# Kernel tuning notes

Hardware: AMD Instinct MI355X
Metric: run time of the kernel (lower is better)

## Reference

```python
import jax, jax.numpy as jnp
import numpy as np

B_, C_, NH_, WS_, HID_ = 8, 512, 16, 7, 2048
HH, WW = 56, 56


def _rel_pos_index(ws):
    coords = np.stack(np.meshgrid(np.arange(ws), np.arange(ws), indexing='ij'))  # (2,ws,ws)
    cf = coords.reshape(2, -1)
    rc = (cf[:, :, None] - cf[:, None, :]).transpose(1, 2, 0)  # (ws2,ws2,2)
    rc[..., 0] += ws - 1
    rc[..., 1] += ws - 1
    rc[..., 0] *= 2 * ws - 1
    return jnp.asarray(rc.sum(-1).reshape(-1))  # (ws2*ws2,)


def _ln(x, g, b, eps):
    mu = x.mean(-1, keepdims=True)
    var = ((x - mu) ** 2).mean(-1, keepdims=True)
    return (x - mu) * jax.lax.rsqrt(var + eps) * g + b


def setup_inputs() -> dict:
    key = jax.random.key(0)
    ks = jax.random.split(key, 8)
    s = lambda k, shape: (jax.random.normal(k, shape, jnp.float32) * 0.02)
    return {
        'x': jax.random.normal(ks[0], (B_, HH * WW, C_), jnp.float32),
        'H': HH, 'W': WW,
        'norm1_g': jnp.ones((C_,), jnp.float32), 'norm1_b': jnp.zeros((C_,), jnp.float32),
        'norm2_g': jnp.ones((C_,), jnp.float32), 'norm2_b': jnp.zeros((C_,), jnp.float32),
        'qkv_w': s(ks[1], (3 * C_, C_)), 'qkv_b': jnp.zeros((3 * C_,), jnp.float32),
        'rpb': s(ks[2], ((2 * WS_ - 1) ** 2, NH_)),
        'fc1_w': s(ks[3], (HID_, C_)), 'fc1_b': jnp.zeros((HID_,), jnp.float32),
        'dw_w': s(ks[4], (HID_, 1, 3, 3)), 'dw_b': jnp.zeros((HID_,), jnp.float32),
        'fc2_w': s(ks[5], (C_, HID_)), 'fc2_b': jnp.zeros((C_,), jnp.float32),
    }


def reference(x, H, W, norm1_g, norm1_b, norm2_g, norm2_b, qkv_w, qkv_b, rpb,
              fc1_w, fc1_b, dw_w, dw_b, fc2_w, fc2_b):
    B, N, C = x.shape
    ws, nh = WS_, NH_
    hd = C // nh
    scale = hd ** -0.5
    ws2 = ws * ws
    nHw, nWw = H // ws, W // ws

    # ---- norm1 + WaveAttention (windowed attention w/ relative position bias) ----
    h = _ln(x, norm1_g, norm1_b, 1e-5)
    qkv = h @ qkv_w.T + qkv_b                                   # [B,N,3C]
    # window partition: [B, nH, ws, nW, ws, 3, nh, hd] -> [3, B*nH*nW, nh, ws2, hd]
    qkv = qkv.reshape(B, nHw, ws, nWw, ws, 3, nh, hd)
    qkv = qkv.transpose(5, 0, 1, 3, 6, 2, 4, 7).reshape(3, B * nHw * nWw, nh, ws2, hd)
    q, k, v = qkv[0], qkv[1], qkv[2]

    attn = jnp.einsum('wnid,wnjd->wnij', q, k) * scale          # [Bw,nh,ws2,ws2]
    bias = rpb[_rel_pos_index(ws)].reshape(ws2, ws2, nh).transpose(2, 0, 1)
    attn = jax.nn.softmax(attn + bias[None], axis=-1)
    out = jnp.einsum('wnij,wnjd->wnid', attn, v)                # [Bw,nh,ws2,hd]
    # window reverse
    out = out.transpose(0, 2, 1, 3).reshape(B, nHw, nWw, ws, ws, C)
    out = out.transpose(0, 1, 3, 2, 4, 5).reshape(B, N, C)
    x = x + out

    # ---- norm2 + PVT2FFN (fc1 -> depthwise 3x3 conv -> GELU -> fc2) ----
    h2 = _ln(x, norm2_g, norm2_b, 1e-5)
    h2 = h2 @ fc1_w.T + fc1_b                                   # [B,N,HID]
    img = h2.reshape(B, H, W, HID_).transpose(0, 3, 1, 2)       # [B,HID,H,W]
    img = jax.lax.conv_general_dilated(img, dw_w, (1, 1), 'SAME',
                                       feature_group_count=HID_)
    img = img + dw_b[None, :, None, None]
    h2 = img.reshape(B, HID_, N).transpose(0, 2, 1)
    h2 = jax.nn.gelu(h2, approximate=False)
    h2 = h2 @ fc2_w.T + fc2_b
    return x + h2
```

## Files before the change

kernel.cpp:

```cpp
#include <hip/hip_runtime.h>
#include <hip/hip_bf16.h>

typedef unsigned short u16;
typedef unsigned int u32;
typedef __attribute__((ext_vector_type(8))) short bf16x8_t;
typedef __attribute__((ext_vector_type(4))) float f32x4_t;
typedef __attribute__((ext_vector_type(8))) u16 u16x8;
typedef __attribute__((ext_vector_type(4))) u32 u32x4;

constexpr int B_  = 8;
constexpr int C_  = 512;
constexpr int NH_ = 16;
constexpr int HID_= 2048;
constexpr int Hh  = 56, Ww = 56;
constexpr int N_  = Hh * Ww;
constexpr int M_  = B_ * N_;

__device__ __forceinline__ u16 f2bf(float f) {
    u32 u = __float_as_uint(f);
    u32 r = (u + 0x7fffu + ((u >> 16) & 1u)) >> 16;
    return (u16)r;
}
__device__ __forceinline__ float bf2f(u16 v) {
    return __uint_as_float(((u32)v) << 16);
}

__device__ __forceinline__ void bar_raw() {
    __asm__ __volatile__("s_barrier" ::: "memory");
}

typedef const void __attribute__((address_space(1))) gvoid_t;
typedef void __attribute__((address_space(3))) lvoid_t;
__device__ __forceinline__ void gload16(const u16* g, u16* l) {
    __builtin_amdgcn_global_load_lds((gvoid_t*)g, (lvoid_t*)l, 16, 0, 0);
}

__global__ void cvt_w(const float* __restrict__ qkvw, const float* __restrict__ fc1w,
                      const float* __restrict__ fc2w, u16* __restrict__ oq,
                      u16* __restrict__ o1, u16* __restrict__ o2) {
    int i = blockIdx.x * 256 + threadIdx.x;
    if (i < 3 * C_ * C_) oq[i] = f2bf(qkvw[i]);
    if (i < HID_ * C_) { o1[i] = f2bf(fc1w[i]); o2[i] = f2bf(fc2w[i]); }
}

__global__ __launch_bounds__(256) void ln_kernel(const float* __restrict__ x,
        const float* __restrict__ g, const float* __restrict__ b, u16* __restrict__ out) {
    int lane = threadIdx.x & 63, wv = threadIdx.x >> 6;
    size_t row = (size_t)blockIdx.x * 4 + wv;
    const float4* xr = (const float4*)(x + row * C_);
    float4 a = xr[lane * 2], c = xr[lane * 2 + 1];
    float s  = a.x + a.y + a.z + a.w + c.x + c.y + c.z + c.w;
    float ss = a.x*a.x + a.y*a.y + a.z*a.z + a.w*a.w + c.x*c.x + c.y*c.y + c.z*c.z + c.w*c.w;
    #pragma unroll
    for (int off = 1; off < 64; off <<= 1) {
        s  += __shfl_xor(s, off);
        ss += __shfl_xor(ss, off);
    }
    float mean = s * (1.0f / C_);
    float var  = ss * (1.0f / C_) - mean * mean;
    float rstd = rsqrtf(var + 1e-5f);
    const float4* g4 = (const float4*)g;
    const float4* b4 = (const float4*)b;
    float4 g0 = g4[lane*2], g1 = g4[lane*2+1], b0 = b4[lane*2], b1 = b4[lane*2+1];
    u16x8 o;
    o[0] = f2bf((a.x - mean) * rstd * g0.x + b0.x);
    o[1] = f2bf((a.y - mean) * rstd * g0.y + b0.y);
    o[2] = f2bf((a.z - mean) * rstd * g0.z + b0.z);
    o[3] = f2bf((a.w - mean) * rstd * g0.w + b0.w);
    o[4] = f2bf((c.x - mean) * rstd * g1.x + b1.x);
    o[5] = f2bf((c.y - mean) * rstd * g1.y + b1.y);
    o[6] = f2bf((c.z - mean) * rstd * g1.z + b1.z);
    o[7] = f2bf((c.w - mean) * rstd * g1.w + b1.w);
    *(u16x8*)&out[row * C_ + lane * 8] = o;
}

template<bool RES, bool OUT_BF16>
__global__ __launch_bounds__(512) void gemm256(
        const u16* __restrict__ A, const u16* __restrict__ B,
        const float* __restrict__ bias, const float* __restrict__ res,
        void* __restrict__ Cout, int M, int N, int K,
        int nbm, int nbn) {
    const int nwg = nbm * nbn;
    const int id = blockIdx.x;
    const int xcd = id & 7, i = id >> 3;
    const int q = nwg >> 3, r = nwg & 7;
    const int gidx = (xcd < r ? xcd * (q + 1) : r * (q + 1) + (xcd - r) * q) + i;
    const int bm = gidx / nbn;
    const int bn = gidx - bm * nbn;

    __shared__ __align__(16) u16 As[2 * 16384];
    __shared__ __align__(16) u16 Bs[2 * 16384];
    const int tid = threadIdx.x;
    const int lane = tid & 63;
    const int w = tid >> 6;
    const int qr = w >> 1, qc = w & 1;

    const int r0 = lane >> 2;
    const int gcb = ((lane & 3) ^ ((lane >> 3) & 3));
    const int fr = lane & 15;
    const int g4 = lane >> 4;
    const int swz = (g4 ^ ((fr >> 1) & 3)) * 8;

    const u16* aBase = A + (size_t)(bm * 256) * K;
    const u16* bBase = B + (size_t)(bn * 256) * K;

    f32x4_t acc[2][2][2][4];
    f32x4_t zero = {0.f, 0.f, 0.f, 0.f};
    #pragma unroll
    for (int a0 = 0; a0 < 2; a0++)
        #pragma unroll
        for (int b0 = 0; b0 < 2; b0++)
            #pragma unroll
            for (int c0 = 0; c0 < 2; c0++)
                #pragma unroll
                for (int d0 = 0; d0 < 4; d0++) acc[a0][b0][c0][d0] = zero;

    auto stage = [&](const u16* gb, u16* lb, int u, int hf) {
        const u16* src = gb + (size_t)(hf * 128 + w * 16 + r0) * K
                            + (size_t)(u * 64 + gcb * 8);
        u16* dst = lb + (u & 1) * 16384 + hf * 8192 + w * 512;
        gload16(src, dst);
        gload16(src + 32, dst + 4096);
    };

    const int NT = K >> 6;
    stage(aBase, As, 0, 0);
    stage(bBase, Bs, 0, 0);
    stage(aBase, As, 0, 1);
    stage(bBase, Bs, 0, 1);
    stage(bBase, Bs, 1, 0);
    stage(aBase, As, 1, 0);
    __asm__ __volatile__("s_waitcnt vmcnt(4)" ::: "memory");
    bar_raw();

    for (int t = 0; t < NT; t++) {
        const int bb = (t & 1) * 16384;
        bf16x8_t bfv[2][4];
        #pragma unroll
        for (int pp = 0; pp < 4; pp++) {
            const int mh = pp & 1, nh = pp >> 1;
            bf16x8_t af[2][2];
            #pragma unroll
            for (int ks = 0; ks < 2; ks++)
                #pragma unroll
                for (int mf = 0; mf < 2; mf++)
                    af[ks][mf] = *(const bf16x8_t*)&As[bb + mh * 8192 + ks * 4096
                                    + (qr * 2 + mf) * 512 + fr * 32 + swz];
            if (pp == 0 || pp == 2) {
                #pragma unroll
                for (int ks = 0; ks < 2; ks++)
                    #pragma unroll
                    for (int nf = 0; nf < 4; nf++)
                        bfv[ks][nf] = *(const bf16x8_t*)&Bs[bb + nh * 8192 + ks * 4096
                                        + (qc * 4 + nf) * 512 + fr * 32 + swz];
            }
            if (pp == 0) {
                if (t + 1 < NT) stage(aBase, As, t + 1, 1);
            } else if (pp == 1) {
                if (t + 1 < NT) stage(bBase, Bs, t + 1, 1);
            } else if (pp == 2) {
                if (t + 2 < NT) stage(bBase, Bs, t + 2, 0);
            } else {
                if (t + 2 < NT) {
                    stage(aBase, As, t + 2, 0);
                    __asm__ __volatile__("s_waitcnt vmcnt(4)" ::: "memory");
                } else if (t + 1 < NT) {
                    __asm__ __volatile__("s_waitcnt vmcnt(0)" ::: "memory");
                }
            }
            bar_raw();
            __asm__ __volatile__("s_waitcnt lgkmcnt(0)" ::: "memory");
            __builtin_amdgcn_s_setprio(1);
            #pragma unroll
            for (int mf = 0; mf < 2; mf++)
                #pragma unroll
                for (int nf = 0; nf < 4; nf++)
                    #pragma unroll
                    for (int ks = 0; ks < 2; ks++)
                        acc[mh][nh][mf][nf] = __builtin_amdgcn_mfma_f32_16x16x32_bf16(
                            af[ks][mf], bfv[ks][nf], acc[mh][nh][mf][nf], 0, 0, 0);
            __builtin_amdgcn_s_setprio(0);
            bar_raw();
        }
    }

    #pragma unroll
    for (int mh = 0; mh < 2; mh++)
        #pragma unroll
        for (int nh = 0; nh < 2; nh++)
            #pragma unroll
            for (int mf = 0; mf < 2; mf++)
                #pragma unroll
                for (int rr = 0; rr < 4; rr++) {
                    int row = bm * 256 + mh * 128 + qr * 32 + mf * 16 + (lane >> 4) * 4 + rr;
                    #pragma unroll
                    for (int nf = 0; nf < 4; nf++) {
                        int col = bn * 256 + nh * 128 + qc * 64 + nf * 16 + (lane & 15);
                        float v = acc[mh][nh][mf][nf][rr] + bias[col];
                        if constexpr (RES) v += res[(size_t)row * N + col];
                        if constexpr (OUT_BF16) ((u16*)Cout)[(size_t)row * N + col] = f2bf(v);
                        else ((float*)Cout)[(size_t)row * N + col] = v;
                    }
                }
}

constexpr int QS = 40;
constexpr int VS = 72;
constexpr int PS = 72;

__global__ __launch_bounds__(256) void attn_kernel(
        const u16* __restrict__ qkv, const float* __restrict__ rpb,
        u16* __restrict__ aout) {
    __shared__ __align__(16) u16 q_s[64 * QS];
    __shared__ __align__(16) u16 k_s[64 * QS];
    __shared__ __align__(16) u16 vT_s[32 * VS];
    __shared__ __align__(16) u16 p_s[64 * PS];
    const int tid = threadIdx.x, lane = tid & 63, wv = tid >> 6;
    const int wh = blockIdx.x;
    const int head = wh & 15, w = wh >> 4;
    const int b = w >> 6, win = w & 63, bh = win >> 3, bw = win & 7;

    {
        int i = tid >> 2, dc = (tid & 3) * 8;
        if (i < 49) {
            int n = (bh * 7 + i / 7) * Ww + (bw * 7 + i % 7);
            const u16* base = qkv + ((size_t)(b * N_ + n)) * (3 * C_) + head * 32 + dc;
            *(u16x8*)&q_s[i * QS + dc] = *(const u16x8*)(base);
            *(u16x8*)&k_s[i * QS + dc] = *(const u16x8*)(base + C_);
        } else {
            u16x8 z = {0,0,0,0,0,0,0,0};
            *(u16x8*)&q_s[i * QS + dc] = z;
            *(u16x8*)&k_s[i * QS + dc] = z;
        }
    }
    for (int f = tid; f < 64 * 32; f += 256) {
        int i = f >> 5, d = f & 31;
        u16 val = 0;
        if (i < 49) {
            int n = (bh * 7 + i / 7) * Ww + (bw * 7 + i % 7);
            val = qkv[((size_t)(b * N_ + n)) * (3 * C_) + 2 * C_ + head * 32 + d];
        }
        vT_s[d * VS + i] = val;
    }
    __syncthreads();

    f32x4_t zero = {0.f, 0.f, 0.f, 0.f};
    f32x4_t s[4];
    bf16x8_t aq = *(const bf16x8_t*)&q_s[(wv * 16 + (lane & 15)) * QS + (lane >> 4) * 8];
    #pragma unroll
    for (int nt = 0; nt < 4; nt++) {
        bf16x8_t bk = *(const bf16x8_t*)&k_s[(nt * 16 + (lane & 15)) * QS + (lane >> 4) * 8];
        s[nt] = __builtin_amdgcn_mfma_f32_16x16x32_bf16(aq, bk, zero, 0, 0, 0);
    }

    const float scale = 0.17677669529663687f;
    #pragma unroll
    for (int r = 0; r < 4; r++) {
        int row = wv * 16 + (lane >> 4) * 4 + r;
        int qy = row / 7, qx = row - qy * 7;
        float pv[4];
        float m = -1e30f;
        #pragma unroll
        for (int nt = 0; nt < 4; nt++) {
            int col = nt * 16 + (lane & 15);
            float bias;
            if (row < 49 && col < 49) {
                int ky = col / 7, kx = col - ky * 7;
                bias = rpb[((qy - ky + 6) * 13 + (qx - kx + 6)) * NH_ + head];
            } else bias = -1e30f;
            float v = s[nt][r] * scale + bias;
            pv[nt] = v;
            m = fmaxf(m, v);
        }
        #pragma unroll
        for (int off = 1; off < 16; off <<= 1) m = fmaxf(m, __shfl_xor(m, off));
        float sum = 0.f;
        #pragma unroll
        for (int nt = 0; nt < 4; nt++) { pv[nt] = __expf(pv[nt] - m); sum += pv[nt]; }
        #pragma unroll
        for (int off = 1; off < 16; off <<= 1) sum += __shfl_xor(sum, off);
        float inv = 1.0f / sum;
        #pragma unroll
        for (int nt = 0; nt < 4; nt++)
            p_s[row * PS + nt * 16 + (lane & 15)] = f2bf(pv[nt] * inv);
    }
    __syncthreads();

    f32x4_t o[2] = {zero, zero};
    #pragma unroll
    for (int kt = 0; kt < 2; kt++) {
        bf16x8_t ap = *(const bf16x8_t*)&p_s[(wv * 16 + (lane & 15)) * PS + kt * 32 + (lane >> 4) * 8];
        #pragma unroll
        for (int nt = 0; nt < 2; nt++) {
            bf16x8_t bv = *(const bf16x8_t*)&vT_s[(nt * 16 + (lane & 15)) * VS + kt * 32 + (lane >> 4) * 8];
            o[nt] = __builtin_amdgcn_mfma_f32_16x16x32_bf16(ap, bv, o[nt], 0, 0, 0);
        }
    }
    u16* obase = aout + ((size_t)(w * 16 + head)) * 49 * 32;
    #pragma unroll
    for (int nt = 0; nt < 2; nt++) {
        #pragma unroll
        for (int r = 0; r < 4; r++) {
            int row = wv * 16 + (lane >> 4) * 4 + r;
            if (row < 49)
                obase[row * 32 + nt * 16 + (lane & 15)] = f2bf(o[nt][r]);
        }
    }
}

__global__ __launch_bounds__(256) void wrev_ln(const float* __restrict__ x,
        const u16* __restrict__ aout, const float* __restrict__ g,
        const float* __restrict__ bt, float* __restrict__ x2, u16* __restrict__ h) {
    int lane = threadIdx.x & 63, wvv = threadIdx.x >> 6;
    int m = blockIdx.x * 4 + wvv;
    int b = m / N_, n = m - b * N_;
    int iy = n / Ww, ix = n - iy * Ww;
    int w = b * 64 + (iy / 7) * 8 + (ix / 7);
    int pos = (iy % 7) * 7 + (ix % 7);
    int head = lane >> 2, d0 = (lane & 3) * 8;
    u16x8 ao = *(const u16x8*)&aout[(((size_t)w * 16 + head) * 49 + pos) * 32 + d0];
    const float4* xr = (const float4*)(x + (size_t)m * C_ + lane * 8);
    float4 a = xr[0], c = xr[1];
    float v[8];
    v[0] = a.x + bf2f(ao[0]); v[1] = a.y + bf2f(ao[1]);
    v[2] = a.z + bf2f(ao[2]); v[3] = a.w + bf2f(ao[3]);
    v[4] = c.x + bf2f(ao[4]); v[5] = c.y + bf2f(ao[5]);
    v[6] = c.z + bf2f(ao[6]); v[7] = c.w + bf2f(ao[7]);
    float s = 0.f, ss = 0.f;
    #pragma unroll
    for (int jj = 0; jj < 8; jj++) { s += v[jj]; ss += v[jj] * v[jj]; }
    #pragma unroll
    for (int off = 1; off < 64; off <<= 1) {
        s  += __shfl_xor(s, off);
        ss += __shfl_xor(ss, off);
    }
    float mean = s * (1.0f / C_);
    float var  = ss * (1.0f / C_) - mean * mean;
    float rstd = rsqrtf(var + 1e-5f);
    float4 o0 = {v[0], v[1], v[2], v[3]}, o1 = {v[4], v[5], v[6], v[7]};
    float4* x2r = (float4*)(x2 + (size_t)m * C_ + lane * 8);
    x2r[0] = o0; x2r[1] = o1;
    const float4* g4 = (const float4*)(g + lane * 8);
    const float4* b4 = (const float4*)(bt + lane * 8);
    float4 g0 = g4[0], g1 = g4[1], bb0 = b4[0], bb1 = b4[1];
    u16x8 o;
    o[0] = f2bf((v[0] - mean) * rstd * g0.x + bb0.x);
    o[1] = f2bf((v[1] - mean) * rstd * g0.y + bb0.y);
    o[2] = f2bf((v[2] - mean) * rstd * g0.z + bb0.z);
    o[3] = f2bf((v[3] - mean) * rstd * g0.w + bb0.w);
    o[4] = f2bf((v[4] - mean) * rstd * g1.x + bb1.x);
    o[5] = f2bf((v[5] - mean) * rstd * g1.y + bb1.y);
    o[6] = f2bf((v[6] - mean) * rstd * g1.z + bb1.z);
    o[7] = f2bf((v[7] - mean) * rstd * g1.w + bb1.w);
    *(u16x8*)&h[(size_t)m * C_ + lane * 8] = o;
}

__global__ __launch_bounds__(256) void dwconv_gelu(const u16* __restrict__ in,
        const float* __restrict__ w, const float* __restrict__ bias, u16* __restrict__ out) {
    const int t = threadIdx.x;
    const int blk = blockIdx.x;
    const int xq = blk & 3;
    const int byp = blk >> 2;
    const int yp = byp % 28;
    const int b = byp / 28;
    const int y0 = yp * 2;
    const int c0 = t * 8;

    float wr[9][8];
    #pragma unroll
    for (int k = 0; k < 9; k++)
        #pragma unroll
        for (int j = 0; j < 8; j++) wr[k][j] = w[(c0 + j) * 9 + k];
    float bs[8];
    #pragma unroll
    for (int j = 0; j < 8; j++) bs[j] = bias[c0 + j];

    u16x8 zerov = {0,0,0,0,0,0,0,0};
    auto ldcol = [&](int xx, u16x8* col) {
        #pragma unroll
        for (int dy = 0; dy < 4; dy++) {
            int yy = y0 + dy - 1;
            bool ok = (yy >= 0 && yy < Hh && xx >= 0 && xx < Ww);
            col[dy] = ok ? *(const u16x8*)&in[(((size_t)b * Hh + yy) * Ww + xx) * HID_ + c0] : zerov;
        }
    };

    int xs = xq * 14;
    u16x8 wA[4], wB[4], wC[4];
    ldcol(xs - 1, wA);
    ldcol(xs, wB);
    for (int x = xs; x < xs + 14; x++) {
        ldcol(x + 1, wC);
        float acc0[8], acc1[8];
        #pragma unroll
        for (int j = 0; j < 8; j++) { acc0[j] = bs[j]; acc1[j] = bs[j]; }
        #pragma unroll
        for (int dy = 0; dy < 3; dy++)
            #pragma unroll
            for (int j = 0; j < 8; j++) {
                acc0[j] += bf2f(wA[dy][j]) * wr[dy * 3 + 0][j];
                acc0[j] += bf2f(wB[dy][j]) * wr[dy * 3 + 1][j];
                acc0[j] += bf2f(wC[dy][j]) * wr[dy * 3 + 2][j];
                acc1[j] += bf2f(wA[dy + 1][j]) * wr[dy * 3 + 0][j];
                acc1[j] += bf2f(wB[dy + 1][j]) * wr[dy * 3 + 1][j];
                acc1[j] += bf2f(wC[dy + 1][j]) * wr[dy * 3 + 2][j];
            }
        u16x8 o0, o1;
        #pragma unroll
        for (int j = 0; j < 8; j++) {
            float v0 = acc0[j];
            o0[j] = f2bf(0.5f * v0 * (1.0f + erff(v0 * 0.70710678118654752f)));
            float v1 = acc1[j];
            o1[j] = f2bf(0.5f * v1 * (1.0f + erff(v1 * 0.70710678118654752f)));
        }
        *(u16x8*)&out[(((size_t)b * Hh + y0) * Ww + x) * HID_ + c0] = o0;
        *(u16x8*)&out[(((size_t)b * Hh + y0 + 1) * Ww + x) * HID_ + c0] = o1;
        #pragma unroll
        for (int dy = 0; dy < 4; dy++) { wA[dy] = wB[dy]; wB[dy] = wC[dy]; }
    }
}

extern "C" void kernel_launch(void* const* d_in, const int* in_sizes, int n_in,
                              void* d_out, int out_size, void* d_ws, size_t ws_size,
                              hipStream_t stream) {
    const float* x    = (const float*)d_in[0];
    const float* n1g  = (const float*)d_in[3];
    const float* n1b  = (const float*)d_in[4];
    const float* n2g  = (const float*)d_in[5];
    const float* n2b  = (const float*)d_in[6];
    const float* qkvw = (const float*)d_in[7];
    const float* qkvb = (const float*)d_in[8];
    const float* rpb  = (const float*)d_in[9];
    const float* fc1w = (const float*)d_in[10];
    const float* fc1b = (const float*)d_in[11];
    const float* dww  = (const float*)d_in[12];
    const float* dwb  = (const float*)d_in[13];
    const float* fc2w = (const float*)d_in[14];
    const float* fc2b = (const float*)d_in[15];

    char* ws = (char*)d_ws;
    float* x2  = (float*)(ws);
    u16*   h   = (u16*)(ws + 51380224);
    u16*   qkvo= (u16*)(ws + 77070336);
    u16*   aout= (u16*)(ws + 154140672);
    u16*   f1o = (u16*)(ws + 154140672);
    u16*   cvo = (u16*)(ws + 51380224);
    u16*   wq  = (u16*)(ws + 256901120);
    u16*   w1  = (u16*)(ws + 256901120 + 1572864);
    u16*   w2  = (u16*)(ws + 256901120 + 1572864 + 2097152);

    cvt_w<<<dim3(4096), dim3(256), 0, stream>>>(qkvw, fc1w, fc2w, wq, w1, w2);
    ln_kernel<<<dim3(M_ / 4), dim3(256), 0, stream>>>(x, n1g, n1b, h);
    gemm256<false, true><<<dim3(588), dim3(512), 0, stream>>>(
        h, wq, qkvb, nullptr, (void*)qkvo, M_, 1536, 512, 98, 6);
    attn_kernel<<<dim3(B_ * 64 * NH_), dim3(256), 0, stream>>>(qkvo, rpb, aout);
    wrev_ln<<<dim3(M_ / 4), dim3(256), 0, stream>>>(x, aout, n2g, n2b, x2, h);
    gemm256<false, true><<<dim3(784), dim3(512), 0, stream>>>(
        h, w1, fc1b, nullptr, (void*)f1o, M_, 2048, 512, 98, 8);
    dwconv_gelu<<<dim3(B_ * 28 * 4), dim3(256), 0, stream>>>(f1o, dww, dwb, cvo);
    gemm256<true, false><<<dim3(196), dim3(512), 0, stream>>>(
        cvo, w2, fc2b, x2, d_out, M_, 512, 2048, 98, 2);
}
```

Before: 523.6 us.

## Remap GEMM warps to 2x4 layout and prefetch LDS fragments across MFMA phases

```diff
diff --git a/kernel.cpp b/kernel.cpp
--- a/kernel.cpp
+++ b/kernel.cpp
@@ -82,9 +82,9 @@
         int nbm, int nbn) {
     const int nwg = nbm * nbn;
     const int id = blockIdx.x;
-    const int xcd = id & 7, i = id >> 3;
+    const int xcd = id & 7, ii = id >> 3;
     const int q = nwg >> 3, r = nwg & 7;
-    const int gidx = (xcd < r ? xcd * (q + 1) : r * (q + 1) + (xcd - r) * q) + i;
+    const int gidx = (xcd < r ? xcd * (q + 1) : r * (q + 1) + (xcd - r) * q) + ii;
     const int bm = gidx / nbn;
     const int bn = gidx - bm * nbn;
 
@@ -93,27 +93,29 @@
     const int tid = threadIdx.x;
     const int lane = tid & 63;
     const int w = tid >> 6;
-    const int qr = w >> 1, qc = w & 1;
+    const int wm = w >> 2, wn = w & 3;
 
     const int r0 = lane >> 2;
     const int gcb = ((lane & 3) ^ ((lane >> 3) & 3));
     const int fr = lane & 15;
     const int g4 = lane >> 4;
     const int swz = (g4 ^ ((fr >> 1) & 3)) * 8;
+    const int bhf = wn >> 1;
+    const int bg0 = (wn & 1) * 4;
 
     const u16* aBase = A + (size_t)(bm * 256) * K;
     const u16* bBase = B + (size_t)(bn * 256) * K;
 
-    f32x4_t acc[2][2][2][4];
+    f32x4_t acc[2][2][4][2];
     f32x4_t zero = {0.f, 0.f, 0.f, 0.f};
     #pragma unroll
     for (int a0 = 0; a0 < 2; a0++)
         #pragma unroll
         for (int b0 = 0; b0 < 2; b0++)
             #pragma unroll
-            for (int c0 = 0; c0 < 2; c0++)
+            for (int c0 = 0; c0 < 4; c0++)
                 #pragma unroll
-                for (int d0 = 0; d0 < 4; d0++) acc[a0][b0][c0][d0] = zero;
+                for (int d0 = 0; d0 < 2; d0++) acc[a0][b0][c0][d0] = zero;
 
     auto stage = [&](const u16* gb, u16* lb, int u, int hf) {
         const u16* src = gb + (size_t)(hf * 128 + w * 16 + r0) * K
@@ -123,80 +125,93 @@
         gload16(src + 32, dst + 4096);
     };
 
+#define RD_A(DST, BB, QM)                                                      \
+    _Pragma("unroll")                                                          \
+    for (int ks = 0; ks < 2; ks++)                                             \
+        _Pragma("unroll")                                                      \
+        for (int mf = 0; mf < 4; mf++)                                         \
+            DST[ks][mf] = *(const bf16x8_t*)&As[(BB) + wm * 8192 + ks * 4096   \
+                            + ((QM) * 4 + mf) * 512 + fr * 32 + swz];
+
+#define RD_B(DST, BB, QN)                                                      \
+    _Pragma("unroll")                                                          \
+    for (int ks = 0; ks < 2; ks++)                                             \
+        _Pragma("unroll")                                                      \
+        for (int nf = 0; nf < 2; nf++)                                         \
+            DST[ks][nf] = *(const bf16x8_t*)&Bs[(BB) + bhf * 8192 + ks * 4096  \
+                            + (bg0 + (QN) * 2 + nf) * 512 + fr * 32 + swz];
+
+#define MMAC(QM, QN, AR, BR)                                                   \
+    __builtin_amdgcn_s_setprio(1);                                             \
+    _Pragma("unroll")                                                          \
+    for (int mf = 0; mf < 4; mf++)                                             \
+        _Pragma("unroll")                                                      \
+        for (int nf = 0; nf < 2; nf++)                                         \
+            _Pragma("unroll")                                                  \
+            for (int ks = 0; ks < 2; ks++)                                     \
+                acc[QM][QN][mf][nf] = __builtin_amdgcn_mfma_f32_16x16x32_bf16( \
+                    AR[ks][mf], BR[ks][nf], acc[QM][QN][mf][nf], 0, 0, 0);     \
+    __builtin_amdgcn_s_setprio(0);
+
     const int NT = K >> 6;
     stage(aBase, As, 0, 0);
+    stage(aBase, As, 0, 1);
     stage(bBase, Bs, 0, 0);
-    stage(aBase, As, 0, 1);
     stage(bBase, Bs, 0, 1);
     stage(bBase, Bs, 1, 0);
     stage(aBase, As, 1, 0);
-    __asm__ __volatile__("s_waitcnt vmcnt(4)" ::: "memory");
+    __asm__ __volatile__("s_waitcnt vmcnt(0)" ::: "memory");
     bar_raw();
+
+    bf16x8_t afr[2][4], bq0[2][2], bq1[2][2];
+    RD_A(afr, 0, 0);
+    RD_B(bq0, 0, 0);
 
     for (int t = 0; t < NT; t++) {
         const int bb = (t & 1) * 16384;
-        bf16x8_t bfv[2][4];
-        #pragma unroll
-        for (int pp = 0; pp < 4; pp++) {
-            const int mh = pp & 1, nh = pp >> 1;
-            bf16x8_t af[2][2];
+        const int ob = bb ^ 16384;
+        MMAC(0, 0, afr, bq0);
+        RD_B(bq1, bb, 1);
+        if (t + 1 < NT) stage(aBase, As, t + 1, 1);
+        bar_raw();
+        MMAC(0, 1, afr, bq1);
+        RD_A(afr, bb, 1);
+        if (t + 1 < NT) stage(bBase, Bs, t + 1, 1);
+        bar_raw();
+        MMAC(1, 1, afr, bq1);
+        if (t + 2 < NT) stage(bBase, Bs, t + 2, 0);
+        bar_raw();
+        MMAC(1, 0, afr, bq0);
+        if (t + 2 < NT) {
+            stage(aBase, As, t + 2, 0);
+            __asm__ __volatile__("s_waitcnt vmcnt(4)" ::: "memory");
+        } else if (t + 1 < NT) {
+            __asm__ __volatile__("s_waitcnt vmcnt(0)" ::: "memory");
+        }
+        bar_raw();
+        if (t + 1 < NT) {
+            RD_A(afr, ob, 0);
+            RD_B(bq0, ob, 0);
+        }
+    }
+
+#undef RD_A
+#undef RD_B
+#undef MMAC
+
+    #pragma unroll
+    for (int qm = 0; qm < 2; qm++)
+        #pragma unroll
+        for (int qn = 0; qn < 2; qn++)
             #pragma unroll
-            for (int ks = 0; ks < 2; ks++)
-                #pragma unroll
-                for (int mf = 0; mf < 2; mf++)
-                    af[ks][mf] = *(const bf16x8_t*)&As[bb + mh * 8192 + ks * 4096
-                                    + (qr * 2 + mf) * 512 + fr * 32 + swz];
-            if (pp == 0 || pp == 2) {
-                #pragma unroll
-                for (int ks = 0; ks < 2; ks++)
-                    #pragma unroll
-                    for (int nf = 0; nf < 4; nf++)
-                        bfv[ks][nf] = *(const bf16x8_t*)&Bs[bb + nh * 8192 + ks * 4096
-                                        + (qc * 4 + nf) * 512 + fr * 32 + swz];
-            }
-            if (pp == 0) {
-                if (t + 1 < NT) stage(aBase, As, t + 1, 1);
-            } else if (pp == 1) {
-                if (t + 1 < NT) stage(bBase, Bs, t + 1, 1);
-            } else if (pp == 2) {
-                if (t + 2 < NT) stage(bBase, Bs, t + 2, 0);
-            } else {
-                if (t + 2 < NT) {
-                    stage(aBase, As, t + 2, 0);
-                    __asm__ __volatile__("s_waitcnt vmcnt(4)" ::: "memory");
-                } else if (t + 1 < NT) {
-                    __asm__ __volatile__("s_waitcnt vmcnt(0)" ::: "memory");
-                }
-            }
-            bar_raw();
-            __asm__ __volatile__("s_waitcnt lgkmcnt(0)" ::: "memory");
-            __builtin_amdgcn_s_setprio(1);
-            #pragma unroll
-            for (int mf = 0; mf < 2; mf++)
-                #pragma unroll
-                for (int nf = 0; nf < 4; nf++)
-                    #pragma unroll
-                    for (int ks = 0; ks < 2; ks++)
-                        acc[mh][nh][mf][nf] = __builtin_amdgcn_mfma_f32_16x16x32_bf16(
-                            af[ks][mf], bfv[ks][nf], acc[mh][nh][mf][nf], 0, 0, 0);
-            __builtin_amdgcn_s_setprio(0);
-            bar_raw();
-        }
-    }
-
-    #pragma unroll
-    for (int mh = 0; mh < 2; mh++)
-        #pragma unroll
-        for (int nh = 0; nh < 2; nh++)
-            #pragma unroll
-            for (int mf = 0; mf < 2; mf++)
+            for (int mf = 0; mf < 4; mf++)
                 #pragma unroll
                 for (int rr = 0; rr < 4; rr++) {
-                    int row = bm * 256 + mh * 128 + qr * 32 + mf * 16 + (lane >> 4) * 4 + rr;
+                    int row = bm * 256 + wm * 128 + qm * 64 + mf * 16 + (lane >> 4) * 4 + rr;
                     #pragma unroll
-                    for (int nf = 0; nf < 4; nf++) {
-                        int col = bn * 256 + nh * 128 + qc * 64 + nf * 16 + (lane & 15);
-                        float v = acc[mh][nh][mf][nf][rr] + bias[col];
+                    for (int nf = 0; nf < 2; nf++) {
+                        int col = bn * 256 + wn * 64 + qn * 32 + nf * 16 + (lane & 15);
+                        float v = acc[qm][qn][mf][nf][rr] + bias[col];
                         if constexpr (RES) v += res[(size_t)row * N + col];
                         if constexpr (OUT_BF16) ((u16*)Cout)[(size_t)row * N + col] = f2bf(v);
                         else ((float*)Cout)[(size_t)row * N + col] = v;
```

Result: faster. 510.1 us (-2.6%).
